# Kernel optimization log

Hardware: AMD Instinct MI355X
Metric: run time of the kernel (lower is better)

The kernel has to match this reference:

```python
import jax, jax.numpy as jnp
import numpy as np

N_NODES = 100000
N_EDGES = 1600000
D_IN = 128
D_HID = 128
D_OUT = 128


def sage_conv(x, src, dst, W_l, b_l, W_r, n_nodes):
    # PyG SAGEConv (mean aggr): out = Linear_l(mean_j x_j) + Linear_r(x_i)
    msg = x[src]                                            # [E, d] gather
    agg = jax.ops.segment_sum(msg, dst, num_segments=n_nodes)  # [N, d]
    cnt = jax.ops.segment_sum(jnp.ones((src.shape[0],), x.dtype), dst,
                              num_segments=n_nodes)
    mean = agg / jnp.maximum(cnt, 1.0)[:, None]             # mean over neighbors
    return mean @ W_l.T + b_l + x @ W_r.T


def setup_inputs() -> dict:
    key = jax.random.key(0)
    ks = jax.random.split(key, 8)
    x = jax.random.normal(ks[0], (N_NODES, D_IN), dtype=jnp.float32)
    edge_index = jax.random.randint(ks[1], (2, N_EDGES), 0, N_NODES, dtype=jnp.int64)
    s1 = 1.0 / np.sqrt(D_IN)
    s2 = 1.0 / np.sqrt(D_HID)
    W1_l = jax.random.uniform(ks[2], (D_HID, D_IN), jnp.float32, -s1, s1)
    b1_l = jax.random.uniform(ks[3], (D_HID,), jnp.float32, -s1, s1)
    W1_r = jax.random.uniform(ks[4], (D_HID, D_IN), jnp.float32, -s1, s1)
    W2_l = jax.random.uniform(ks[5], (D_OUT, D_HID), jnp.float32, -s2, s2)
    b2_l = jax.random.uniform(ks[6], (D_OUT,), jnp.float32, -s2, s2)
    W2_r = jax.random.uniform(ks[7], (D_OUT, D_HID), jnp.float32, -s2, s2)
    return {"x": x, "edge_index": edge_index, "W1_l": W1_l, "b1_l": b1_l,
            "W1_r": W1_r, "W2_l": W2_l, "b2_l": b2_l, "W2_r": W2_r}


def reference(x, edge_index, W1_l, b1_l, W1_r, W2_l, b2_l, W2_r):
    src, dst = edge_index[0], edge_index[1]
    n = x.shape[0]
    h = sage_conv(x, src, dst, W1_l, b1_l, W1_r, n)
    h = jax.nn.relu(h)
    # F.dropout with training=False (eval mode) is identity
    out = sage_conv(h, src, dst, W2_l, b2_l, W2_r, n)
    return out
```

## Files before the change

kernel.cpp:

```cpp
#include <hip/hip_runtime.h>

typedef __attribute__((ext_vector_type(8))) short short8;
typedef __attribute__((ext_vector_type(4))) float f32x4;
typedef __attribute__((ext_vector_type(2))) float f32x2;

#define NBMAX 512
#define CAP 8192

__device__ inline unsigned short f2bf(float f) {
  union { float f; unsigned u; } v; v.f = f;
  unsigned r = v.u + 0x7fffu + ((v.u >> 16) & 1u);
  return (unsigned short)(r >> 16);
}

__device__ inline void addf2(f32x2 (&a)[4], uint4 v) {
  union { uint2 u; f32x2 f; } t;
  t.u.x = v.x << 16; t.u.y = v.x & 0xffff0000u; a[0] += t.f;
  t.u.x = v.y << 16; t.u.y = v.y & 0xffff0000u; a[1] += t.f;
  t.u.x = v.z << 16; t.u.y = v.z & 0xffff0000u; a[2] += t.f;
  t.u.x = v.w << 16; t.u.y = v.w & 0xffff0000u; a[3] += t.f;
}

__device__ inline int load_src(const int* ei, int E, int e, int f64) {
  return f64 ? ei[2 * e] : ei[e];
}
__device__ inline int load_dst(const int* ei, int E, int e, int f64) {
  return f64 ? ei[2 * (E + e)] : ei[E + e];
}

__global__ __launch_bounds__(256) void prep(
    const int* __restrict__ ei, int E,
    int* __restrict__ btot, unsigned* __restrict__ stage, int SB,
    const float* __restrict__ x, unsigned short* __restrict__ xb, int n8,
    const float* __restrict__ W1l, const float* __restrict__ W1r,
    const float* __restrict__ W2l, const float* __restrict__ W2r,
    unsigned short* __restrict__ Wp) {
  __shared__ int lcnt[NBMAX];
  __shared__ int lbase[NBMAX];
  __shared__ int sflag;
  const int b = blockIdx.x;
  const int t = threadIdx.x;

  if (b < SB) {
    if (t == 0) sflag = 0;
    for (int i = t; i < NBMAX; i += 256) lcnt[i] = 0;
    __syncthreads();
    const int e0 = b * 2048;
    {
      int e = e0 + t;
      int v = (e < E) ? ei[2 * e + 1] : 0;
      if (v) atomicOr(&sflag, 1);
    }
    __syncthreads();
    const int f64 = (sflag == 0) ? 1 : 0;

    unsigned pk[8];
    int bks[8];
#pragma unroll
    for (int i = 0; i < 8; ++i) {
      int e = e0 + i * 256 + t;
      if (e < E) {
        int s = load_src(ei, E, e, f64);
        int d = load_dst(ei, E, e, f64);
        pk[i] = ((unsigned)s << 8) | ((unsigned)d & 255u);
        bks[i] = d >> 8;
        atomicAdd(&lcnt[d >> 8], 1);
      } else {
        bks[i] = -1;
      }
    }
    __syncthreads();
    for (int i = t; i < NBMAX; i += 256) {
      int c = lcnt[i];
      lbase[i] = c ? atomicAdd(&btot[i], c) : 0;
    }
    __syncthreads();
    for (int i = t; i < NBMAX; i += 256) lcnt[i] = 0;
    __syncthreads();
#pragma unroll
    for (int i = 0; i < 8; ++i) {
      int bk = bks[i];
      if (bk >= 0) {
        int r = atomicAdd(&lcnt[bk], 1);
        stage[(size_t)bk * CAP + lbase[bk] + r] = pk[i];
      }
    }
    return;
  }

  if (b < SB + 4) {
    const int m = b - SB;
    const float* W = (m == 0) ? W1l : (m == 1) ? W1r : (m == 2) ? W2l : W2r;
    unsigned short* dst = Wp + (size_t)m * 16384;
#pragma unroll
    for (int it = 0; it < 8; ++it) {
      int id = it * 256 + t;
      int j = id >> 4;
      int kc = id & 15;
      int s = kc >> 2, q = kc & 3;
      int jt = j >> 4, nn2 = j & 15;
      int c = (s * 8 + jt) * 4 + q;
      const float* src = W + j * 128 + kc * 8;
      union { unsigned short u[8]; uint4 v; } tv;
#pragma unroll
      for (int k = 0; k < 8; ++k) tv.u[k] = f2bf(src[k]);
      *(uint4*)(dst + (c * 16 + nn2) * 8) = tv.v;
    }
    return;
  }

  const int cb = b - SB - 4;
  const int nxb = gridDim.x - SB - 4;
  int i = cb * 256 + t;
  const int stride = nxb * 256;
  for (; i < n8; i += stride) {
    float4 v0 = ((const float4*)x)[2 * i];
    float4 v1 = ((const float4*)x)[2 * i + 1];
    union { unsigned short u[8]; uint4 v; } tv;
    tv.u[0] = f2bf(v0.x); tv.u[1] = f2bf(v0.y);
    tv.u[2] = f2bf(v0.z); tv.u[3] = f2bf(v0.w);
    tv.u[4] = f2bf(v1.x); tv.u[5] = f2bf(v1.y);
    tv.u[6] = f2bf(v1.z); tv.u[7] = f2bf(v1.w);
    ((uint4*)xb)[i] = tv.v;
  }
}

__global__ __launch_bounds__(256) void bucket_fill2(
    const unsigned* __restrict__ stage, const int* __restrict__ btot,
    int* __restrict__ offs, int* __restrict__ cnt, float* __restrict__ inv,
    int* __restrict__ csr, int N) {
  __shared__ int lhist[256];
  __shared__ int lscan[256];
  __shared__ int lcur[256];
  __shared__ int red[256];
  const int b = blockIdx.x;
  const int t = threadIdx.x;
  int sum = 0;
  for (int j = t; j < b; j += 256) sum += btot[j];
  red[t] = sum;
  lhist[t] = 0;
  __syncthreads();
  for (int d = 128; d; d >>= 1) {
    if (t < d) red[t] += red[t + d];
    __syncthreads();
  }
  const int base = red[0];
  const int count = btot[b];
  const unsigned* sp = stage + (size_t)b * CAP;
  for (int i = t; i < count; i += 256)
    atomicAdd(&lhist[sp[i] & 255u], 1);
  __syncthreads();
  int v = lhist[t];
  lscan[t] = v;
  __syncthreads();
  for (int d = 1; d < 256; d <<= 1) {
    int tv = (t >= d) ? lscan[t - d] : 0;
    __syncthreads();
    lscan[t] += tv;
    __syncthreads();
  }
  const int excl = lscan[t] - v;
  const int node = b * 256 + t;
  if (node < N) {
    offs[node] = base + excl;
    cnt[node] = v;
    inv[node] = 1.0f / (float)((v > 1) ? v : 1);
  }
  lcur[t] = base + excl;
  __syncthreads();
  for (int i = t; i < count; i += 256) {
    unsigned sd = sp[i];
    int p = atomicAdd(&lcur[sd & 255u], 1);
    csr[p] = (int)(sd >> 8);
  }
}

__global__ __launch_bounds__(256, 4) void agg_mean(
    const unsigned short* __restrict__ A, const float* __restrict__ inv,
    const int* __restrict__ offs, const int* __restrict__ cnt,
    const int* __restrict__ csr, unsigned short* __restrict__ M, int n) {
  int pr = (int)((blockIdx.x * 256 + threadIdx.x) >> 6);
  int n0 = pr * 2;
  if (n0 >= n) return;
  const int n1 = n0 + 1;
  const bool has1 = (n1 < n);
  const int lane = threadIdx.x & 63;
  const int g = lane >> 4;
  const int l = lane & 15;
  const int deg0 = cnt[n0];
  const int deg1 = has1 ? cnt[n1] : 0;
  const int start = offs[n0];
  const int T = deg0 + deg1;
  f32x2 acc0[4] = {{0.f, 0.f}, {0.f, 0.f}, {0.f, 0.f}, {0.f, 0.f}};
  f32x2 acc1[4] = {{0.f, 0.f}, {0.f, 0.f}, {0.f, 0.f}, {0.f, 0.f}};
  const char* Ab = (const char*)A + (size_t)l * 16;

  if (T <= 64) {
    int offb = ((lane < T) ? csr[start + lane] : 0) << 8;
    const bool twoB = (T > 32);
    int nbA[8], nbB[8];
    uint4 vA[8], vB[8];
#pragma unroll
    for (int j = 0; j < 8; ++j) nbA[j] = __shfl(offb, j * 4 + g);
    if (twoB) {
#pragma unroll
      for (int j = 0; j < 8; ++j) nbB[j] = __shfl(offb, 32 + j * 4 + g);
    }
#pragma unroll
    for (int j = 0; j < 8; ++j)
      vA[j] = *(const uint4*)(Ab + (size_t)(unsigned)nbA[j]);
    if (twoB) {
#pragma unroll
      for (int j = 0; j < 8; ++j)
        vB[j] = *(const uint4*)(Ab + (size_t)(unsigned)nbB[j]);
    }
#pragma unroll
    for (int j = 0; j < 8; ++j) {
      int e = j * 4 + g;
      if (e < deg0) addf2(acc0, vA[j]);
      else if (e < T) addf2(acc1, vA[j]);
    }
    if (twoB) {
#pragma unroll
      for (int j = 0; j < 8; ++j) {
        int e = 32 + j * 4 + g;
        if (e < deg0) addf2(acc0, vB[j]);
        else if (e < T) addf2(acc1, vB[j]);
      }
    }
  } else {
    for (int node = 0; node < 2; ++node) {
      int dg = node ? deg1 : deg0;
      int st = node ? (start + deg0) : start;
      for (int base = 0; base < dg; base += 64) {
        int m = dg - base;
        if (m > 64) m = 64;
        int offb = ((lane < m) ? csr[st + base + lane] : 0) << 8;
#pragma unroll 4
        for (int i = 0; i < m; i += 4) {
          int sl = i + g;
          int nbv = __shfl(offb, sl & 63);
          if (sl < m) {
            uint4 v = *(const uint4*)(Ab + (size_t)(unsigned)nbv);
            if (node) addf2(acc1, v);
            else addf2(acc0, v);
          }
        }
      }
    }
  }

#pragma unroll
  for (int k = 0; k < 4; ++k) {
    acc0[k].x += __shfl_xor(acc0[k].x, 16);
    acc0[k].x += __shfl_xor(acc0[k].x, 32);
    acc0[k].y += __shfl_xor(acc0[k].y, 16);
    acc0[k].y += __shfl_xor(acc0[k].y, 32);
    acc1[k].x += __shfl_xor(acc1[k].x, 16);
    acc1[k].x += __shfl_xor(acc1[k].x, 32);
    acc1[k].y += __shfl_xor(acc1[k].y, 16);
    acc1[k].y += __shfl_xor(acc1[k].y, 32);
  }

  const int c0 = l * 8 + g * 2;
  {
    float s = inv[n0];
    unsigned pkt = (unsigned)f2bf(acc0[g].x * s) |
                   ((unsigned)f2bf(acc0[g].y * s) << 16);
    *(unsigned*)(M + (size_t)n0 * 128 + c0) = pkt;
  }
  if (has1) {
    float s = inv[n1];
    unsigned pkt = (unsigned)f2bf(acc1[g].x * s) |
                   ((unsigned)f2bf(acc1[g].y * s) << 16);
    *(unsigned*)(M + (size_t)n1 * 128 + c0) = pkt;
  }
}

template <int RELU, int OUTBF>
__global__ __launch_bounds__(256) void gemm_fused(
    const unsigned short* __restrict__ Am,
    const unsigned short* __restrict__ As,
    const unsigned short* __restrict__ Wp,
    const float* __restrict__ bias, void* __restrict__ outp, int n) {
  __shared__ unsigned short wsh[2 * 16384];
  const int tid = threadIdx.x;

  {
    const uint4* wsrc = (const uint4*)Wp;
    uint4* wdst = (uint4*)wsh;
#pragma unroll
    for (int it = 0; it < 16; ++it) {
      int id = it * 256 + tid;
      wdst[id] = wsrc[id];
    }
  }
  __syncthreads();

  const int lane = tid & 63;
  const int wave = tid >> 6;
  const int nn = lane & 15;
  const int quad = lane >> 4;
  const int rowbase = blockIdx.x * 64 + wave * 16;

  int nodeA = rowbase + nn;
  if (nodeA > n - 1) nodeA = n - 1;

  short8 am[4], asf[4];
#pragma unroll
  for (int s = 0; s < 4; ++s) {
    am[s] = *(const short8*)(Am + (size_t)nodeA * 128 + s * 32 + quad * 8);
    asf[s] = *(const short8*)(As + (size_t)nodeA * 128 + s * 32 + quad * 8);
  }

  f32x4 acc[8];
#pragma unroll
  for (int jt = 0; jt < 8; ++jt) acc[jt] = (f32x4){0.f, 0.f, 0.f, 0.f};

#pragma unroll
  for (int jt = 0; jt < 8; ++jt) {
#pragma unroll
    for (int s = 0; s < 4; ++s) {
      int c = (s * 8 + jt) * 4 + quad;
      short8 bl = *(const short8*)(wsh + (c * 16 + nn) * 8);
      short8 br = *(const short8*)(wsh + 16384 + (c * 16 + nn) * 8);
      acc[jt] = __builtin_amdgcn_mfma_f32_16x16x32_bf16(am[s], bl, acc[jt], 0, 0, 0);
      acc[jt] = __builtin_amdgcn_mfma_f32_16x16x32_bf16(asf[s], br, acc[jt], 0, 0, 0);
    }
  }

#pragma unroll
  for (int jt = 0; jt < 8; ++jt) {
    int col = jt * 16 + nn;
    float bv = bias[col];
#pragma unroll
    for (int r = 0; r < 4; ++r) {
      int ro = rowbase + quad * 4 + r;
      if (ro < n) {
        float o = acc[jt][r] + bv;
        if (RELU) o = fmaxf(o, 0.f);
        if (OUTBF) {
          ((unsigned short*)outp)[(size_t)ro * 128 + col] = f2bf(o);
        } else {
          ((float*)outp)[(size_t)ro * 128 + col] = o;
        }
      }
    }
  }
}


extern "C" void kernel_launch(void* const* d_in, const int* in_sizes, int n_in,
                              void* d_out, int out_size, void* d_ws, size_t ws_size,
                              hipStream_t stream) {
  const float* x = (const float*)d_in[0];
  const int* ei = (const int*)d_in[1];
  const float* W1l = (const float*)d_in[2];
  const float* b1 = (const float*)d_in[3];
  const float* W1r = (const float*)d_in[4];
  const float* W2l = (const float*)d_in[5];
  const float* b2 = (const float*)d_in[6];
  const float* W2r = (const float*)d_in[7];
  float* out = (float*)d_out;

  const int N = in_sizes[0] / 128;
  const int E = in_sizes[1] / 2;
  const int nb = (N + 255) / 256;

  char* p = (char*)d_ws;
  auto alloc = [&](size_t bytes) {
    char* r = p;
    p += (bytes + 255) & ~(size_t)255;
    return r;
  };
  int* btot = (int*)alloc((size_t)NBMAX * 4);
  int* cnt = (int*)alloc((size_t)N * 4);
  int* offs = (int*)alloc((size_t)N * 4);
  float* inv = (float*)alloc((size_t)N * 4);
  int* csr = (int*)alloc((size_t)E * 4);
  unsigned short* Mb = (unsigned short*)alloc((size_t)N * 128 * 2);
  unsigned short* Wpb = (unsigned short*)alloc((size_t)4 * 16384 * 2);
  size_t stage_bytes = (size_t)nb * CAP * 4;
  size_t hb_bytes = (size_t)N * 128 * 2;
  char* shared_region = alloc(stage_bytes > hb_bytes ? stage_bytes : hb_bytes);
  unsigned short* hb = (unsigned short*)shared_region;
  unsigned* stage = (unsigned*)shared_region;

  unsigned short* xb = (unsigned short*)d_out;

  hipMemsetAsync(btot, 0, (size_t)nb * 4, stream);

  const int SB = (E + 2047) / 2048;
  prep<<<SB + 4 + 2048, 256, 0, stream>>>(ei, E, btot, stage, SB,
                                          x, xb, N * 128 / 8,
                                          W1l, W1r, W2l, W2r, Wpb);
  bucket_fill2<<<nb, 256, 0, stream>>>(stage, btot, offs, cnt, inv, csr, N);

  const int gb = (N + 63) / 64;
  const int pairs = (N + 1) / 2;
  const int ab2 = (pairs + 3) / 4;

  agg_mean<<<ab2, 256, 0, stream>>>(xb, inv, offs, cnt, csr, Mb, N);
  gemm_fused<1, 1><<<gb, 256, 0, stream>>>(Mb, xb, Wpb, b1, (void*)hb, N);
  agg_mean<<<ab2, 256, 0, stream>>>(hb, inv, offs, cnt, csr, Mb, N);
  gemm_fused<0, 0><<<gb, 256, 0, stream>>>(Mb, hb, Wpb + 32768, b2, (void*)out, N);
}
```

Measured before the change: 343.1 us.

## Persistent GEMM blocks, larger prep edge chunks, split gather register sets

The fused GEMM becomes persistent: at most 512 blocks loop over the 64-row chunks, so the 64KB weight copy into shared memory happens once per block instead of once per chunk. The prep kernel now handles 4096 edges per block instead of 2048, halving the global atomics on the bucket totals. The aggregation gather for degree up to 64 is split into two scoped phases so they do not hold 16 uint4 loads live together, lowering register pressure at the cost of less memory-level parallelism. The persistent grid can lose occupancy or load balance if 512 blocks do not fill the device.

```diff
diff --git a/kernel.cpp b/kernel.cpp
--- a/kernel.cpp
+++ b/kernel.cpp
@@ -45,7 +45,7 @@
     if (t == 0) sflag = 0;
     for (int i = t; i < NBMAX; i += 256) lcnt[i] = 0;
     __syncthreads();
-    const int e0 = b * 2048;
+    const int e0 = b * 4096;
     {
       int e = e0 + t;
       int v = (e < E) ? ei[2 * e + 1] : 0;
@@ -54,10 +54,10 @@
     __syncthreads();
     const int f64 = (sflag == 0) ? 1 : 0;
 
-    unsigned pk[8];
-    int bks[8];
-#pragma unroll
-    for (int i = 0; i < 8; ++i) {
+    unsigned pk[16];
+    int bks[16];
+#pragma unroll
+    for (int i = 0; i < 16; ++i) {
       int e = e0 + i * 256 + t;
       if (e < E) {
         int s = load_src(ei, E, e, f64);
@@ -78,7 +78,7 @@
     for (int i = t; i < NBMAX; i += 256) lcnt[i] = 0;
     __syncthreads();
 #pragma unroll
-    for (int i = 0; i < 8; ++i) {
+    for (int i = 0; i < 16; ++i) {
       int bk = bks[i];
       if (bk >= 0) {
         int r = atomicAdd(&lcnt[bk], 1);
@@ -197,35 +197,34 @@
 
   if (T <= 64) {
     int offb = ((lane < T) ? csr[start + lane] : 0) << 8;
-    const bool twoB = (T > 32);
-    int nbA[8], nbB[8];
-    uint4 vA[8], vB[8];
-#pragma unroll
-    for (int j = 0; j < 8; ++j) nbA[j] = __shfl(offb, j * 4 + g);
-    if (twoB) {
-#pragma unroll
-      for (int j = 0; j < 8; ++j) nbB[j] = __shfl(offb, 32 + j * 4 + g);
-    }
-#pragma unroll
-    for (int j = 0; j < 8; ++j)
-      vA[j] = *(const uint4*)(Ab + (size_t)(unsigned)nbA[j]);
-    if (twoB) {
+    {
+      int nb2[8];
+      uint4 vv[8];
+#pragma unroll
+      for (int j = 0; j < 8; ++j) nb2[j] = __shfl(offb, j * 4 + g);
 #pragma unroll
       for (int j = 0; j < 8; ++j)
-        vB[j] = *(const uint4*)(Ab + (size_t)(unsigned)nbB[j]);
-    }
-#pragma unroll
-    for (int j = 0; j < 8; ++j) {
-      int e = j * 4 + g;
-      if (e < deg0) addf2(acc0, vA[j]);
-      else if (e < T) addf2(acc1, vA[j]);
-    }
-    if (twoB) {
+        vv[j] = *(const uint4*)(Ab + (size_t)(unsigned)nb2[j]);
+#pragma unroll
+      for (int j = 0; j < 8; ++j) {
+        int e = j * 4 + g;
+        if (e < deg0) addf2(acc0, vv[j]);
+        else if (e < T) addf2(acc1, vv[j]);
+      }
+    }
+    if (T > 32) {
+      int nb2[8];
+      uint4 vv[8];
+#pragma unroll
+      for (int j = 0; j < 8; ++j) nb2[j] = __shfl(offb, 32 + j * 4 + g);
+#pragma unroll
+      for (int j = 0; j < 8; ++j)
+        vv[j] = *(const uint4*)(Ab + (size_t)(unsigned)nb2[j]);
 #pragma unroll
       for (int j = 0; j < 8; ++j) {
         int e = 32 + j * 4 + g;
-        if (e < deg0) addf2(acc0, vB[j]);
-        else if (e < T) addf2(acc1, vB[j]);
+        if (e < deg0) addf2(acc0, vv[j]);
+        else if (e < T) addf2(acc1, vv[j]);
       }
     }
   } else {
@@ -282,7 +281,8 @@
     const unsigned short* __restrict__ Am,
     const unsigned short* __restrict__ As,
     const unsigned short* __restrict__ Wp,
-    const float* __restrict__ bias, void* __restrict__ outp, int n) {
+    const float* __restrict__ bias, void* __restrict__ outp, int n,
+    int nchunks) {
   __shared__ unsigned short wsh[2 * 16384];
   const int tid = threadIdx.x;
 
@@ -301,48 +301,50 @@
   const int wave = tid >> 6;
   const int nn = lane & 15;
   const int quad = lane >> 4;
-  const int rowbase = blockIdx.x * 64 + wave * 16;
-
-  int nodeA = rowbase + nn;
-  if (nodeA > n - 1) nodeA = n - 1;
-
-  short8 am[4], asf[4];
-#pragma unroll
-  for (int s = 0; s < 4; ++s) {
-    am[s] = *(const short8*)(Am + (size_t)nodeA * 128 + s * 32 + quad * 8);
-    asf[s] = *(const short8*)(As + (size_t)nodeA * 128 + s * 32 + quad * 8);
-  }
-
-  f32x4 acc[8];
-#pragma unroll
-  for (int jt = 0; jt < 8; ++jt) acc[jt] = (f32x4){0.f, 0.f, 0.f, 0.f};
-
-#pragma unroll
-  for (int jt = 0; jt < 8; ++jt) {
+
+  for (int ch = blockIdx.x; ch < nchunks; ch += gridDim.x) {
+    const int rowbase = ch * 64 + wave * 16;
+    int nodeA = rowbase + nn;
+    if (nodeA > n - 1) nodeA = n - 1;
+
+    short8 am[4], asf[4];
 #pragma unroll
     for (int s = 0; s < 4; ++s) {
-      int c = (s * 8 + jt) * 4 + quad;
-      short8 bl = *(const short8*)(wsh + (c * 16 + nn) * 8);
-      short8 br = *(const short8*)(wsh + 16384 + (c * 16 + nn) * 8);
-      acc[jt] = __builtin_amdgcn_mfma_f32_16x16x32_bf16(am[s], bl, acc[jt], 0, 0, 0);
-      acc[jt] = __builtin_amdgcn_mfma_f32_16x16x32_bf16(asf[s], br, acc[jt], 0, 0, 0);
-    }
-  }
-
-#pragma unroll
-  for (int jt = 0; jt < 8; ++jt) {
-    int col = jt * 16 + nn;
-    float bv = bias[col];
-#pragma unroll
-    for (int r = 0; r < 4; ++r) {
-      int ro = rowbase + quad * 4 + r;
-      if (ro < n) {
-        float o = acc[jt][r] + bv;
-        if (RELU) o = fmaxf(o, 0.f);
-        if (OUTBF) {
-          ((unsigned short*)outp)[(size_t)ro * 128 + col] = f2bf(o);
-        } else {
-          ((float*)outp)[(size_t)ro * 128 + col] = o;
+      am[s] = *(const short8*)(Am + (size_t)nodeA * 128 + s * 32 + quad * 8);
+      asf[s] = *(const short8*)(As + (size_t)nodeA * 128 + s * 32 + quad * 8);
+    }
+
+    f32x4 acc[8];
+#pragma unroll
+    for (int jt = 0; jt < 8; ++jt) acc[jt] = (f32x4){0.f, 0.f, 0.f, 0.f};
+
+#pragma unroll
+    for (int jt = 0; jt < 8; ++jt) {
+#pragma unroll
+      for (int s = 0; s < 4; ++s) {
+        int c = (s * 8 + jt) * 4 + quad;
+        short8 bl = *(const short8*)(wsh + (c * 16 + nn) * 8);
+        short8 br = *(const short8*)(wsh + 16384 + (c * 16 + nn) * 8);
+        acc[jt] = __builtin_amdgcn_mfma_f32_16x16x32_bf16(am[s], bl, acc[jt], 0, 0, 0);
+        acc[jt] = __builtin_amdgcn_mfma_f32_16x16x32_bf16(asf[s], br, acc[jt], 0, 0, 0);
+      }
+    }
+
+#pragma unroll
+    for (int jt = 0; jt < 8; ++jt) {
+      int col = jt * 16 + nn;
+      float bv = bias[col];
+#pragma unroll
+      for (int r = 0; r < 4; ++r) {
+        int ro = rowbase + quad * 4 + r;
+        if (ro < n) {
+          float o = acc[jt][r] + bv;
+          if (RELU) o = fmaxf(o, 0.f);
+          if (OUTBF) {
+            ((unsigned short*)outp)[(size_t)ro * 128 + col] = f2bf(o);
+          } else {
+            ((float*)outp)[(size_t)ro * 128 + col] = o;
+          }
         }
       }
     }
@@ -390,18 +392,19 @@
 
   hipMemsetAsync(btot, 0, (size_t)nb * 4, stream);
 
-  const int SB = (E + 2047) / 2048;
+  const int SB = (E + 4095) / 4096;
   prep<<<SB + 4 + 2048, 256, 0, stream>>>(ei, E, btot, stage, SB,
                                           x, xb, N * 128 / 8,
                                           W1l, W1r, W2l, W2r, Wpb);
   bucket_fill2<<<nb, 256, 0, stream>>>(stage, btot, offs, cnt, inv, csr, N);
 
   const int gb = (N + 63) / 64;
+  const int PB = gb < 512 ? gb : 512;
   const int pairs = (N + 1) / 2;
   const int ab2 = (pairs + 3) / 4;
 
   agg_mean<<<ab2, 256, 0, stream>>>(xb, inv, offs, cnt, csr, Mb, N);
-  gemm_fused<1, 1><<<gb, 256, 0, stream>>>(Mb, xb, Wpb, b1, (void*)hb, N);
+  gemm_fused<1, 1><<<PB, 256, 0, stream>>>(Mb, xb, Wpb, b1, (void*)hb, N, gb);
   agg_mean<<<ab2, 256, 0, stream>>>(hb, inv, offs, cnt, csr, Mb, N);
-  gemm_fused<0, 0><<<gb, 256, 0, stream>>>(Mb, hb, Wpb + 32768, b2, (void*)out, N);
-}
+  gemm_fused<0, 0><<<PB, 256, 0, stream>>>(Mb, hb, Wpb + 32768, b2, (void*)out, N, gb);
+}
```

Result: faster. 310.8 us (-9.4%).
